# Optimization experiments

Hardware: AMD Instinct MI355X
Metric: run time of the kernel (lower is better)

Reference implementation:

```python
import jax, jax.numpy as jnp
import numpy as np

N_NODES = 100000
N_REL = 8
N_EDGES = 100000  # per relation
DIM = 128


def setup_inputs() -> dict:
    key = jax.random.key(0)
    ks = jax.random.split(key, 8)
    s = 1.0 / np.sqrt(DIM)
    return {
        "entity_embeddings": jax.random.normal(ks[0], (N_NODES, DIM), jnp.float32),
        "edge_index": jax.random.randint(ks[1], (N_REL, 2, N_EDGES), 0, N_NODES, jnp.int32),
        "edge_weights": jax.random.uniform(ks[2], (N_REL, N_EDGES), jnp.float32),
        "relW1": jax.random.normal(ks[3], (N_REL, DIM, DIM), jnp.float32) * s,
        "selfW1": jax.random.normal(ks[4], (DIM, DIM), jnp.float32) * s,
        "bias1": jnp.zeros((N_REL, DIM), jnp.float32),
        "relW2": jax.random.normal(ks[5], (N_REL, DIM, DIM), jnp.float32) * s,
        "selfW2": jax.random.normal(ks[6], (DIM, DIM), jnp.float32) * s,
        "bias2": jnp.zeros((N_REL, DIM), jnp.float32),
    }


def _wrgcn_layer(x, edge_index, edge_weights, relW, selfW, bias):
    # x: [N, Din]; edge_index: [R, 2, E]; edge_weights: [R, E]
    N = x.shape[0]
    R, _, E = edge_index.shape
    src = edge_index[:, 0]  # [R, E]
    tgt = edge_index[:, 1]  # [R, E]
    # gather -> per-relation matmul -> edge-weight scale
    src_emb = x[src]  # [R, E, Din]
    msg = jnp.einsum('red,rdo->reo', src_emb, relW) * edge_weights[..., None]  # [R, E, Dout]
    # scatter-add to target nodes (shared node space across relations)
    agg = jax.ops.segment_sum(msg.reshape(R * E, -1), tgt.reshape(R * E), num_segments=N)
    # bias added once per (relation, unique target node)
    tgt_mask = jnp.zeros((R, N), x.dtype).at[jnp.arange(R)[:, None], tgt].set(1.0)  # [R, N]
    agg = agg + jnp.einsum('rn,ro->no', tgt_mask, bias)
    # self loop
    return agg + x @ selfW


def reference(entity_embeddings, edge_index, edge_weights,
              relW1, selfW1, bias1, relW2, selfW2, bias2):
    h = _wrgcn_layer(entity_embeddings, edge_index, edge_weights, relW1, selfW1, bias1)
    h = jax.nn.relu(h)  # dropout is identity in eval mode
    out = _wrgcn_layer(h, edge_index, edge_weights, relW2, selfW2, bias2)
    return out
```

## Files before the change

### kernel.cpp

```cpp
#include <hip/hip_runtime.h>
#include <hip/hip_bf16.h>

#define NN 100000
#define DD 128
#define RR 8
#define EE 100000
#define NP1 (NN + 1)
#define NB1 98
#define PADN (NB1 * 1024)
#define SEG 8
#define WPR (NN / SEG)

typedef __attribute__((ext_vector_type(8))) short short8;
typedef __attribute__((ext_vector_type(4))) float f32x4;

__device__ __forceinline__ unsigned short f2bf(float v) {
  union { float f; unsigned int u; } x; x.f = v;
  unsigned int r = (x.u + 0x7FFFu + ((x.u >> 16) & 1u)) >> 16;
  return (unsigned short)r;
}

__global__ void k_cast4(const float* __restrict__ src, unsigned short* __restrict__ dst, int n4) {
  int i = blockIdx.x * blockDim.x + threadIdx.x;
  int stride = gridDim.x * blockDim.x;
  for (; i < n4; i += stride) {
    float4 v = reinterpret_cast<const float4*>(src)[i];
    ushort4 o;
    o.x = f2bf(v.x); o.y = f2bf(v.y); o.z = f2bf(v.z); o.w = f2bf(v.w);
    reinterpret_cast<ushort4*>(dst)[i] = o;
  }
}

__global__ void k_castT2(const float* __restrict__ s1, unsigned short* __restrict__ d1,
                         const float* __restrict__ s2, unsigned short* __restrict__ d2,
                         int total) {
  int i = blockIdx.x * blockDim.x + threadIdx.x;
  if (i >= total) return;
  const float* src = blockIdx.y ? s2 : s1;
  unsigned short* dst = blockIdx.y ? d2 : d1;
  int r = i >> 14;
  int k = (i >> 7) & 127;
  int o = i & 127;
  dst[(r << 14) + (o << 7) + k] = f2bf(src[i]);
}

__global__ void k_zero2(unsigned int* __restrict__ p1, int n1,
                        unsigned int* __restrict__ p2, int n2) {
  int i = blockIdx.x * blockDim.x + threadIdx.x;
  if (i < n1) p1[i] = 0u;
  else if (i - n1 < n2) p2[i - n1] = 0u;
}

__global__ void k_hist_mask(const int* __restrict__ edge_index, int* __restrict__ cnt,
                            unsigned int* __restrict__ mb) {
  int e = blockIdx.x * blockDim.x + threadIdx.x;
  int r = blockIdx.y;
  if (e >= EE) return;
  int tgt = edge_index[(size_t)r * 2 * EE + EE + e];
  atomicAdd(&cnt[r * PADN + tgt], 1);
  atomicOr(&mb[tgt], 1u << r);
}

__global__ void k_scan1(const int* __restrict__ cnt, int* __restrict__ start, int* __restrict__ bsum) {
  const int r = blockIdx.y, b = blockIdx.x, t = threadIdx.x;
  const int bin0 = b * 1024 + t * 4;
  int4 c = *reinterpret_cast<const int4*>(&cnt[r * PADN + bin0]);
  int s1 = c.x, s2 = s1 + c.y, s3 = s2 + c.z, tot = s3 + c.w;
  __shared__ int sh[256];
  sh[t] = tot;
  __syncthreads();
  for (int off = 1; off < 256; off <<= 1) {
    int v = (t >= off) ? sh[t - off] : 0;
    __syncthreads();
    sh[t] += v;
    __syncthreads();
  }
  int excl = sh[t] - tot;
  if (t == 255) bsum[r * NB1 + b] = sh[255];
  const int base = r * NP1;
  if (bin0 < NN) start[base + bin0] = excl;
  if (bin0 + 1 < NN) start[base + bin0 + 1] = excl + s1;
  if (bin0 + 2 < NN) start[base + bin0 + 2] = excl + s2;
  if (bin0 + 3 < NN) start[base + bin0 + 3] = excl + s3;
}

__global__ void k_scan2(const int* __restrict__ bsum, int* __restrict__ boff, int* __restrict__ start) {
  const int r = blockIdx.x, t = threadIdx.x;
  int v = (t < NB1) ? bsum[r * NB1 + t] : 0;
  __shared__ int sh[128];
  sh[t] = v;
  __syncthreads();
  for (int off = 1; off < 128; off <<= 1) {
    int u = (t >= off) ? sh[t - off] : 0;
    __syncthreads();
    sh[t] += u;
    __syncthreads();
  }
  if (t < NB1) boff[r * NB1 + t] = sh[t] - v;
  if (t == 0) start[r * NP1 + NN] = EE;
}

__global__ void k_scan3(int* __restrict__ start, const int* __restrict__ boff, int* __restrict__ cursor) {
  const int r = blockIdx.y, b = blockIdx.x, t = threadIdx.x;
  const int bin0 = b * 1024 + t * 4;
  const int off = boff[r * NB1 + b];
  const int base = r * NP1;
#pragma unroll
  for (int k = 0; k < 4; ++k) {
    int bin = bin0 + k;
    if (bin < NN) {
      int v = start[base + bin] + off;
      start[base + bin] = v;
      cursor[r * NN + bin] = v;
    }
  }
}

__global__ void k_scatter2(const int* __restrict__ edge_index, const float* __restrict__ ew,
                           int* __restrict__ cursor, int2* __restrict__ es) {
  int e = blockIdx.x * blockDim.x + threadIdx.x;
  int r = blockIdx.y;
  if (e >= EE) return;
  const int* src_p = edge_index + (size_t)r * 2 * EE;
  int tgt = src_p[EE + e];
  int pos = atomicAdd(&cursor[r * NN + tgt], 1);
  es[(size_t)r * EE + pos] = make_int2(src_p[e], __float_as_int(ew[(size_t)r * EE + e]));
}


__device__ __forceinline__ void preagg_wave(const unsigned short* __restrict__ Xsrc,
                                            const int2* __restrict__ es,
                                            const int* __restrict__ start,
                                            int r, int n0, int lane,
                                            float (&a0)[SEG], float (&a1)[SEG]) {
  const size_t rEE = (size_t)r * EE;
  int b = start[r * NP1 + n0 + (lane < 8 ? lane : 8)];
  int p[SEG + 1];
#pragma unroll
  for (int i = 0; i <= SEG; ++i) p[i] = __builtin_amdgcn_readlane(b, i);
#pragma unroll
  for (int i = 0; i < SEG; ++i) { a0[i] = 0.f; a1[i] = 0.f; }
  const int p0 = p[0];
  const int count = p[SEG] - p0;
  if (count <= 0) return;
  int rounds = 0;
#pragma unroll
  for (int i = 0; i < SEG; ++i) rounds = max(rounds, p[i + 1] - p[i]);
  const unsigned int* Xu = reinterpret_cast<const unsigned int*>(Xsrc);

  if (count <= 64) {
    int wl = lane < count ? lane : count - 1;
    int2 ew = es[rEE + p0 + wl];
    int esrc = ew.x;
    int ewbits = ew.y;
    for (int j = 0; j < rounds; ++j) {
#pragma unroll
      for (int i = 0; i < SEG; ++i) {
        int pos = p[i] + j;
        if (pos < p[i + 1]) {
          int widx = pos - p0;
          int s = __builtin_amdgcn_readlane(esrc, widx);
          float wv = __int_as_float(__builtin_amdgcn_readlane(ewbits, widx));
          unsigned int d = Xu[(size_t)s * 64 + lane];
          union { unsigned int u; float f; } lo, hi;
          lo.u = d << 16;
          hi.u = d & 0xFFFF0000u;
          a0[i] += wv * lo.f;
          a1[i] += wv * hi.f;
        }
      }
    }
  } else {
    for (int j = 0; j < rounds; ++j) {
#pragma unroll
      for (int i = 0; i < SEG; ++i) {
        int pos = p[i] + j;
        if (pos < p[i + 1]) {
          int2 e = es[rEE + pos];
          float wv = __int_as_float(e.y);
          unsigned int d = Xu[(size_t)e.x * 64 + lane];
          union { unsigned int u; float f; } lo, hi;
          lo.u = d << 16;
          hi.u = d & 0xFFFF0000u;
          a0[i] += wv * lo.f;
          a1[i] += wv * hi.f;
        }
      }
    }
  }
}

__launch_bounds__(256, 4)
__global__ void k_preagg_seg3(const unsigned short* __restrict__ Xsrc,
                              const int2* __restrict__ es, const int* __restrict__ start,
                              unsigned short* __restrict__ P0, unsigned short* __restrict__ P1,
                              unsigned short* __restrict__ P2,
                              int rbase, int nrel) {
  const int wid = blockIdx.x * 4 + (threadIdx.x >> 6);
  if (wid >= nrel * WPR) return;
  const int lane = threadIdx.x & 63;
  const int rr = wid / WPR;
  const int n0 = (wid - rr * WPR) * SEG;
  float a0[SEG], a1[SEG];
  preagg_wave(Xsrc, es, start, rbase + rr, n0, lane, a0, a1);
  unsigned short* P = (rr == 0) ? P0 : ((rr == 1) ? P1 : P2);
  unsigned int* Pw = reinterpret_cast<unsigned int*>(P);
#pragma unroll
  for (int i = 0; i < SEG; ++i)
    Pw[(size_t)(n0 + i) * 64 + lane] = (unsigned int)f2bf(a0[i]) | ((unsigned int)f2bf(a1[i]) << 16);
}

__launch_bounds__(256, 4)
__global__ void k_preagg_seg8(const unsigned short* __restrict__ Xsrc,
                              const int2* __restrict__ es, const int* __restrict__ start,
                              unsigned short* __restrict__ P0, unsigned short* __restrict__ Pws) {
  const int wid = blockIdx.x * 4 + (threadIdx.x >> 6);
  if (wid >= RR * WPR) return;
  const int lane = threadIdx.x & 63;
  const int rr = wid / WPR;
  const int n0 = (wid - rr * WPR) * SEG;
  float a0[SEG], a1[SEG];
  preagg_wave(Xsrc, es, start, rr, n0, lane, a0, a1);
  unsigned short* P = (rr == 0) ? P0 : (Pws + (size_t)(rr - 1) * NN * DD);
  unsigned int* Pw = reinterpret_cast<unsigned int*>(P);
#pragma unroll
  for (int i = 0; i < SEG; ++i)
    Pw[(size_t)(n0 + i) * 64 + lane] = (unsigned int)f2bf(a0[i]) | ((unsigned int)f2bf(a1[i]) << 16);
}


typedef const __attribute__((address_space(1))) void* gas1_t;
typedef __attribute__((address_space(3))) void* las3_t;

__device__ __forceinline__ void gl16(const void* g, void* s) {
  __builtin_amdgcn_global_load_lds((gas1_t)g, (las3_t)s, 16, 0, 0);
}

template <bool CLAMP>
__device__ __forceinline__ void stage_lds(const unsigned short* __restrict__ g,
                                          unsigned short* lds, int t, int row0) {
  const int w = t >> 6, l = t & 63;
  const int sub = l >> 4, s = l & 15;
#pragma unroll
  for (int c = 0; c < 8; ++c) {
    int rowblk = c * 16 + w * 4;
    int row = rowblk + sub;
    int grow = row0 + row;
    int sr = CLAMP ? (grow < NN ? grow : NN - 1) : grow;
    const unsigned short* src = g + (size_t)sr * 128 + ((s ^ (row & 7)) << 3);
    gl16(src, lds + rowblk * 128);
  }
}

__device__ __forceinline__ void mfma_tile(const unsigned short* __restrict__ lA,
                                          const unsigned short* __restrict__ lB,
                                          f32x4 (&acc)[2][8], int w, int l) {
  const int lrow = l & 15, kgrp = l >> 4;
#pragma unroll
  for (int ks = 0; ks < 4; ++ks) {
    int kc = ks * 4 + kgrp;
    int ra = w * 32 + lrow;
    int rb = ra + 16;
    short8 a0 = *reinterpret_cast<const short8*>(&lA[(ra << 7) + ((kc ^ (ra & 7)) << 3)]);
    short8 a1 = *reinterpret_cast<const short8*>(&lA[(rb << 7) + ((kc ^ (rb & 7)) << 3)]);
#pragma unroll
    for (int ct = 0; ct < 8; ++ct) {
      int ro = ct * 16 + lrow;
      short8 b = *reinterpret_cast<const short8*>(&lB[(ro << 7) + ((kc ^ (ro & 7)) << 3)]);
      acc[0][ct] = __builtin_amdgcn_mfma_f32_16x16x32_bf16(a0, b, acc[0][ct], 0, 0, 0);
      acc[1][ct] = __builtin_amdgcn_mfma_f32_16x16x32_bf16(a1, b, acc[1][ct], 0, 0, 0);
    }
  }
}

template <bool L1>
__launch_bounds__(256, 2)
__global__ void k_gemm_fused(const unsigned short* __restrict__ Aself,
                             const unsigned short* __restrict__ Wself,
                             const unsigned short* __restrict__ P0,
                             const unsigned short* __restrict__ Pws,
                             const unsigned short* __restrict__ Wrel,
                             const unsigned int* __restrict__ maskbits,
                             const float* __restrict__ bias,
                             void* __restrict__ outp) {
  __shared__ __align__(16) unsigned short lA[128 * 128];
  __shared__ __align__(16) unsigned short lB[128 * 128];
  const int t = threadIdx.x;
  const int row0 = blockIdx.x * 128;
  const int w = t >> 6, l = t & 63;
  const int lrow = l & 15, kgrp = l >> 4;
  f32x4 acc[2][8] = {};

  stage_lds<true>(Aself, lA, t, row0);
  stage_lds<false>(Wself, lB, t, 0);
  __syncthreads();
  mfma_tile(lA, lB, acc, w, l);
#pragma unroll 1
  for (int r = 0; r < RR; ++r) {
    const unsigned short* Pr = (r == 0) ? P0 : (Pws + (size_t)(r - 1) * NN * DD);
    __syncthreads();
    stage_lds<true>(Pr, lA, t, row0);
    stage_lds<false>(Wrel + (r << 14), lB, t, 0);
    __syncthreads();
    mfma_tile(lA, lB, acc, w, l);
  }

  {
    short8 a0 = {}, a1 = {}, bf[8];
#pragma unroll
    for (int ct = 0; ct < 8; ++ct) bf[ct] = short8{};
    if (kgrp == 0) {
      int ra = row0 + w * 32 + lrow;
      int rb = ra + 16;
      unsigned int ma = (ra < NN) ? maskbits[ra] : 0u;
      unsigned int mb = (rb < NN) ? maskbits[rb] : 0u;
#pragma unroll
      for (int k = 0; k < 8; ++k) {
        a0[k] = (short)(((ma >> k) & 1u) ? 0x3F80 : 0);
        a1[k] = (short)(((mb >> k) & 1u) ? 0x3F80 : 0);
      }
#pragma unroll
      for (int ct = 0; ct < 8; ++ct) {
        int o = ct * 16 + lrow;
#pragma unroll
        for (int k = 0; k < 8; ++k) bf[ct][k] = (short)f2bf(bias[k * 128 + o]);
      }
    }
#pragma unroll
    for (int ct = 0; ct < 8; ++ct) {
      acc[0][ct] = __builtin_amdgcn_mfma_f32_16x16x32_bf16(a0, bf[ct], acc[0][ct], 0, 0, 0);
      acc[1][ct] = __builtin_amdgcn_mfma_f32_16x16x32_bf16(a1, bf[ct], acc[1][ct], 0, 0, 0);
    }
  }

#pragma unroll
  for (int rt = 0; rt < 2; ++rt) {
#pragma unroll
    for (int j = 0; j < 4; ++j) {
      int grow = row0 + w * 32 + rt * 16 + kgrp * 4 + j;
      if (grow < NN) {
        if (L1) {
          unsigned short* op = (unsigned short*)outp + (size_t)grow * 128 + lrow;
#pragma unroll
          for (int ct = 0; ct < 8; ++ct) op[ct * 16] = f2bf(fmaxf(acc[rt][ct][j], 0.f));
        } else {
          float* op = (float*)outp + (size_t)grow * 128 + lrow;
#pragma unroll
          for (int ct = 0; ct < 8; ++ct) op[ct * 16] = acc[rt][ct][j];
        }
      }
    }
  }
}

template <int NT>
__launch_bounds__(256, 2)
__global__ void k_gemm_multi(const unsigned short* __restrict__ A0, const unsigned short* __restrict__ W0,
                             const unsigned short* __restrict__ A1, const unsigned short* __restrict__ W1,
                             const unsigned short* __restrict__ A2, const unsigned short* __restrict__ W2,
                             const unsigned short* __restrict__ A3, const unsigned short* __restrict__ W3,
                             float* __restrict__ outp, int accum) {
  __shared__ __align__(16) unsigned short lA[128 * 128];
  __shared__ __align__(16) unsigned short lB[128 * 128];
  const int t = threadIdx.x;
  const int row0 = blockIdx.x * 128;
  const int w = t >> 6, l = t & 63;
  const int lrow = l & 15, kgrp = l >> 4;
  f32x4 acc[2][8] = {};

  const unsigned short* As[4] = {A0, A1, A2, A3};
  const unsigned short* Ws[4] = {W0, W1, W2, W3};
#pragma unroll
  for (int term = 0; term < NT; ++term) {
    if (term) __syncthreads();
    stage_lds<true>(As[term], lA, t, row0);
    stage_lds<false>(Ws[term], lB, t, 0);
    __syncthreads();
    mfma_tile(lA, lB, acc, w, l);
  }

#pragma unroll
  for (int rt = 0; rt < 2; ++rt) {
#pragma unroll
    for (int j = 0; j < 4; ++j) {
      int grow = row0 + w * 32 + rt * 16 + kgrp * 4 + j;
      if (grow < NN) {
        float* op = outp + (size_t)grow * 128 + lrow;
        if (accum) {
#pragma unroll
          for (int ct = 0; ct < 8; ++ct) op[ct * 16] += acc[rt][ct][j];
        } else {
#pragma unroll
          for (int ct = 0; ct < 8; ++ct) op[ct * 16] = acc[rt][ct][j];
        }
      }
    }
  }
}

__global__ void k_epi1(const float* __restrict__ h32, const unsigned int* __restrict__ maskbits,
                       const float* __restrict__ bias, unsigned short* __restrict__ hb) {
  int gid = blockIdx.x * blockDim.x + threadIdx.x;
  if (gid >= NN * 32) return;
  int n = gid >> 5, c = (gid & 31) << 2;
  float4 v = *reinterpret_cast<const float4*>(h32 + (size_t)n * 128 + c);
  unsigned int mb = maskbits[n];
  float b0 = 0, b1 = 0, b2 = 0, b3 = 0;
#pragma unroll
  for (int r = 0; r < RR; ++r) {
    if ((mb >> r) & 1u) {
      const float* bp = bias + r * 128 + c;
      b0 += bp[0]; b1 += bp[1]; b2 += bp[2]; b3 += bp[3];
    }
  }
  ushort4 o;
  o.x = f2bf(fmaxf(v.x + b0, 0.f));
  o.y = f2bf(fmaxf(v.y + b1, 0.f));
  o.z = f2bf(fmaxf(v.z + b2, 0.f));
  o.w = f2bf(fmaxf(v.w + b3, 0.f));
  *reinterpret_cast<ushort4*>(hb + (size_t)n * 128 + c) = o;
}

__global__ void k_epi2(float* __restrict__ out, const unsigned int* __restrict__ maskbits,
                       const float* __restrict__ bias) {
  int gid = blockIdx.x * blockDim.x + threadIdx.x;
  if (gid >= NN * 32) return;
  int n = gid >> 5, c = (gid & 31) << 2;
  unsigned int mb = maskbits[n];
  if (!mb) return;
  float b0 = 0, b1 = 0, b2 = 0, b3 = 0;
#pragma unroll
  for (int r = 0; r < RR; ++r) {
    if ((mb >> r) & 1u) {
      const float* bp = bias + r * 128 + c;
      b0 += bp[0]; b1 += bp[1]; b2 += bp[2]; b3 += bp[3];
    }
  }
  float* p = out + (size_t)n * 128 + c;
  float4 v = *reinterpret_cast<const float4*>(p);
  v.x += b0; v.y += b1; v.z += b2; v.w += b3;
  *reinterpret_cast<float4*>(p) = v;
}

extern "C" void kernel_launch(void* const* d_in, const int* in_sizes, int n_in,
                              void* d_out, int out_size, void* d_ws, size_t ws_size,
                              hipStream_t stream) {
  const float* X   = (const float*)d_in[0];
  const int*   EI  = (const int*)d_in[1];
  const float* EW  = (const float*)d_in[2];
  const float* rW1 = (const float*)d_in[3];
  const float* sW1 = (const float*)d_in[4];
  const float* b1  = (const float*)d_in[5];
  const float* rW2 = (const float*)d_in[6];
  const float* sW2 = (const float*)d_in[7];
  const float* b2  = (const float*)d_in[8];
  float* out = (float*)d_out;
  char* ws = (char*)d_ws;

  size_t off = 0;
  auto take = [&](size_t sz) { char* p = ws + off; off += (sz + 255) & ~(size_t)255; return p; };
  unsigned short* Xb   = (unsigned short*)take((size_t)NN * DD * 2);
  unsigned short* hb   = (unsigned short*)take((size_t)NN * DD * 2);
  unsigned int*  maskb = (unsigned int*)take((size_t)NN * 4);
  unsigned short* rW1t = (unsigned short*)take((size_t)RR * DD * DD * 2);
  unsigned short* sW1t = (unsigned short*)take((size_t)DD * DD * 2);
  unsigned short* rW2t = (unsigned short*)take((size_t)RR * DD * DD * 2);
  unsigned short* sW2t = (unsigned short*)take((size_t)DD * DD * 2);
  int*   cnt    = (int*)take((size_t)RR * PADN * 4);
  int*   start  = (int*)take((size_t)RR * NP1 * 4);
  int*   cursor = (int*)take((size_t)RR * NN * 4);
  int*   bsum   = (int*)take((size_t)RR * NB1 * 4);
  int*   boff   = (int*)take((size_t)RR * NB1 * 4);
  int2*  es     = (int2*)take((size_t)RR * EE * 8);

  const size_t szReg = ((size_t)NN * DD * 2 + 255) & ~(size_t)255;
  const bool bigA = (off + 7 * szReg <= ws_size);
  unsigned short* Pws = nullptr;
  float* h32 = nullptr;
  if (bigA) {
    Pws = (unsigned short*)take(7 * szReg);
  } else {
    h32 = (float*)take((size_t)NN * DD * 4);
  }

  k_cast4<<<2048, 256, 0, stream>>>(X, Xb, NN * DD / 4);
  k_castT2<<<dim3((RR * DD * DD + 255) / 256, 2), 256, 0, stream>>>(rW1, rW1t, rW2, rW2t, RR * DD * DD);
  k_castT2<<<dim3((DD * DD + 255) / 256, 2), 256, 0, stream>>>(sW1, sW1t, sW2, sW2t, DD * DD);

  k_zero2<<<(NN + RR * PADN + 255) / 256, 256, 0, stream>>>(maskb, NN, (unsigned int*)cnt, RR * PADN);
  k_hist_mask<<<dim3((EE + 255) / 256, RR), 256, 0, stream>>>(EI, cnt, maskb);
  k_scan1<<<dim3(NB1, RR), 256, 0, stream>>>(cnt, start, bsum);
  k_scan2<<<RR, 128, 0, stream>>>(bsum, boff, start);
  k_scan3<<<dim3(NB1, RR), 256, 0, stream>>>(start, boff, cursor);
  k_scatter2<<<dim3((EE + 255) / 256, RR), 256, 0, stream>>>(EI, EW, cursor, es);

  const int nblk = (NN + 127) / 128;
  unsigned short* outu = (unsigned short*)d_out;

  if (bigA) {
    const int pblk = (RR * WPR + 3) / 4;
    k_preagg_seg8<<<pblk, 256, 0, stream>>>(Xb, es, start, outu, Pws);
    k_gemm_fused<true><<<nblk, 256, 0, stream>>>(Xb, sW1t, outu, Pws, rW1t, maskb, b1, hb);
    k_preagg_seg8<<<pblk, 256, 0, stream>>>(hb, es, start, Xb, Pws);
    k_gemm_fused<false><<<nblk, 256, 0, stream>>>(hb, sW2t, Xb, Pws, rW2t, maskb, b2, out);
  } else {
    unsigned short* h32u = (unsigned short*)h32;
    const int pblk3 = (3 * WPR + 3) / 4;
    const int pblk2 = (2 * WPR + 3) / 4;
    {
      unsigned short* P0 = outu;
      unsigned short* P1 = outu + (size_t)NN * DD;
      unsigned short* P2 = hb;
      k_preagg_seg3<<<pblk3, 256, 0, stream>>>(Xb, es, start, P0, P1, P2, 0, 3);
      k_gemm_multi<4><<<nblk, 256, 0, stream>>>(Xb, sW1t, P0, rW1t, P1, rW1t + (1 << 14), P2, rW1t + (2 << 14), h32, 0);
      k_preagg_seg3<<<pblk3, 256, 0, stream>>>(Xb, es, start, P0, P1, P2, 3, 3);
      k_gemm_multi<3><<<nblk, 256, 0, stream>>>(P0, rW1t + (3 << 14), P1, rW1t + (4 << 14), P2, rW1t + (5 << 14), nullptr, nullptr, h32, 1);
      k_preagg_seg3<<<pblk2, 256, 0, stream>>>(Xb, es, start, P0, P1, P2, 6, 2);
      k_gemm_multi<2><<<nblk, 256, 0, stream>>>(P0, rW1t + (6 << 14), P1, rW1t + (7 << 14), nullptr, nullptr, nullptr, nullptr, h32, 1);
    }
    k_epi1<<<(NN * 32 + 255) / 256, 256, 0, stream>>>(h32, maskb, b1, hb);
    {
      unsigned short* P0 = h32u;
      unsigned short* P1 = h32u + (size_t)NN * DD;
      unsigned short* P2 = Xb;
      k_preagg_seg3<<<pblk3, 256, 0, stream>>>(hb, es, start, P0, P1, P2, 0, 3);
      k_gemm_multi<4><<<nblk, 256, 0, stream>>>(hb, sW2t, P0, rW2t, P1, rW2t + (1 << 14), P2, rW2t + (2 << 14), out, 0);
      k_preagg_seg3<<<pblk3, 256, 0, stream>>>(hb, es, start, P0, P1, P2, 3, 3);
      k_gemm_multi<3><<<nblk, 256, 0, stream>>>(P0, rW2t + (3 << 14), P1, rW2t + (4 << 14), P2, rW2t + (5 << 14), nullptr, nullptr, out, 1);
      k_preagg_seg3<<<pblk2, 256, 0, stream>>>(hb, es, start, P0, P1, P2, 6, 2);
      k_gemm_multi<2><<<nblk, 256, 0, stream>>>(P0, rW2t + (6 << 14), P1, rW2t + (7 << 14), nullptr, nullptr, nullptr, nullptr, out, 1);
    }
    k_epi2<<<(NN * 32 + 255) / 256, 256, 0, stream>>>(out, maskb, b2);
  }
}
```

Before: 408.6 us.

## Double-buffer GEMM LDS staging in K-halves to overlap loads with MFMA

The fused GEMM now splits each 128-wide K tile into two 64-wide halves and double-buffers them in LDS. The global-to-LDS load for the next half is issued before the MFMAs on the current half, and the loop needs one barrier per stage instead of two. This is meant to hide load latency behind compute across the 9 terms. LDS use per block stays the same, but there are twice as many stage steps and the swizzle addressing changes.

New measurement: 426.9 us. +4.5%, slower.

```diff
diff --git a/kernel.cpp b/kernel.cpp
--- a/kernel.cpp
+++ b/kernel.cpp
@@ -126,7 +126,6 @@
   int pos = atomicAdd(&cursor[r * NN + tgt], 1);
   es[(size_t)r * EE + pos] = make_int2(src_p[e], __float_as_int(ew[(size_t)r * EE + e]));
 }
-
 
 __device__ __forceinline__ void preagg_wave(const unsigned short* __restrict__ Xsrc,
                                             const int2* __restrict__ es,
@@ -228,12 +227,49 @@
     Pw[(size_t)(n0 + i) * 64 + lane] = (unsigned int)f2bf(a0[i]) | ((unsigned int)f2bf(a1[i]) << 16);
 }
 
-
 typedef const __attribute__((address_space(1))) void* gas1_t;
 typedef __attribute__((address_space(3))) void* las3_t;
 
 __device__ __forceinline__ void gl16(const void* g, void* s) {
   __builtin_amdgcn_global_load_lds((gas1_t)g, (las3_t)s, 16, 0, 0);
+}
+
+template <bool CLAMP>
+__device__ __forceinline__ void stage_half(const unsigned short* __restrict__ g,
+                                           unsigned short* lds, int t, int row0, int half) {
+  const int w = t >> 6, l = t & 63;
+  const int sub = l >> 3;
+  const int sl = l & 7;
+#pragma unroll
+  for (int c = 0; c < 4; ++c) {
+    int rb8 = c * 32 + w * 8;
+    int row = rb8 + sub;
+    int grow = row0 + row;
+    int sr = CLAMP ? (grow < NN ? grow : NN - 1) : grow;
+    const unsigned short* src = g + (size_t)sr * 128 + half * 64 + ((sl ^ (row & 7)) << 3);
+    gl16(src, lds + rb8 * 64);
+  }
+}
+
+__device__ __forceinline__ void mfma_half(const unsigned short* __restrict__ lA,
+                                          const unsigned short* __restrict__ lB,
+                                          f32x4 (&acc)[2][8], int w, int l) {
+  const int lrow = l & 15, kgrp = l >> 4;
+#pragma unroll
+  for (int ks = 0; ks < 2; ++ks) {
+    int kc = ks * 4 + kgrp;
+    int ra = w * 32 + lrow;
+    int rb = ra + 16;
+    short8 a0 = *reinterpret_cast<const short8*>(&lA[(ra << 6) + ((kc ^ (ra & 7)) << 3)]);
+    short8 a1 = *reinterpret_cast<const short8*>(&lA[(rb << 6) + ((kc ^ (rb & 7)) << 3)]);
+#pragma unroll
+    for (int ct = 0; ct < 8; ++ct) {
+      int ro = ct * 16 + lrow;
+      short8 b = *reinterpret_cast<const short8*>(&lB[(ro << 6) + ((kc ^ (ro & 7)) << 3)]);
+      acc[0][ct] = __builtin_amdgcn_mfma_f32_16x16x32_bf16(a0, b, acc[0][ct], 0, 0, 0);
+      acc[1][ct] = __builtin_amdgcn_mfma_f32_16x16x32_bf16(a1, b, acc[1][ct], 0, 0, 0);
+    }
+  }
 }
 
 template <bool CLAMP>
@@ -283,26 +319,36 @@
                              const unsigned int* __restrict__ maskbits,
                              const float* __restrict__ bias,
                              void* __restrict__ outp) {
-  __shared__ __align__(16) unsigned short lA[128 * 128];
-  __shared__ __align__(16) unsigned short lB[128 * 128];
+  __shared__ __align__(16) unsigned short lA[2][128 * 64];
+  __shared__ __align__(16) unsigned short lB[2][128 * 64];
   const int t = threadIdx.x;
   const int row0 = blockIdx.x * 128;
   const int w = t >> 6, l = t & 63;
   const int lrow = l & 15, kgrp = l >> 4;
   f32x4 acc[2][8] = {};
 
-  stage_lds<true>(Aself, lA, t, row0);
-  stage_lds<false>(Wself, lB, t, 0);
+  auto A_of = [&](int term) -> const unsigned short* {
+    return term == 0 ? Aself : (term == 1 ? P0 : Pws + (size_t)(term - 2) * NN * DD);
+  };
+  auto B_of = [&](int term) -> const unsigned short* {
+    return term == 0 ? Wself : Wrel + ((term - 1) << 14);
+  };
+
+  stage_half<true>(A_of(0), lA[0], t, row0, 0);
+  stage_half<false>(B_of(0), lB[0], t, 0, 0);
   __syncthreads();
-  mfma_tile(lA, lB, acc, w, l);
+
+  int cur = 0;
 #pragma unroll 1
-  for (int r = 0; r < RR; ++r) {
-    const unsigned short* Pr = (r == 0) ? P0 : (Pws + (size_t)(r - 1) * NN * DD);
+  for (int st = 0; st < 18; ++st) {
+    if (st < 17) {
+      int nt = (st + 1) >> 1, nh = (st + 1) & 1;
+      stage_half<true>(A_of(nt), lA[cur ^ 1], t, row0, nh);
+      stage_half<false>(B_of(nt), lB[cur ^ 1], t, 0, nh);
+    }
+    mfma_half(lA[cur], lB[cur], acc, w, l);
     __syncthreads();
-    stage_lds<true>(Pr, lA, t, row0);
-    stage_lds<false>(Wrel + (r << 14), lB, t, 0);
-    __syncthreads();
-    mfma_tile(lA, lB, acc, w, l);
+    cur ^= 1;
   }
 
   {
```
